# Kernel tuning notes

Hardware: AMD Instinct MI355X
Metric: run time of the kernel (lower is better)

Reference implementation:

```python
import jax, jax.numpy as jnp
import numpy as np

N = 2060          # drug-graph nodes (m_drug_d_num)
F_OUT = 901       # out_feats, forced by Linear(901*2, ...)
M = 901 + (N - 1183)  # 1778 fused node rows
E = N * 64
N_TRAIN, N_TEST = 100000, 30000
EPS = 1e-5


def setup_inputs() -> dict:
    key = jax.random.key(0)
    ks = jax.random.split(key, 30)
    f32 = jnp.float32
    inp = {
        'x_feat': jax.random.normal(ks[0], (N, N), f32),
        'mirna_feat': jax.random.normal(ks[1], (M, F_OUT), f32),
        'Wg': jax.random.normal(ks[2], (N, F_OUT), f32) * 0.02,
        'att_src': jax.random.normal(ks[3], (F_OUT,), f32) * 0.05,
        'att_dst': jax.random.normal(ks[4], (F_OUT,), f32) * 0.05,
        'gat_b': jnp.zeros((F_OUT,), f32),
        'lw1': jax.random.normal(ks[5], (1, 2), f32) * 0.5,
        'lb1': jnp.zeros((1,), f32),
        'lw2': jax.random.normal(ks[6], (2, 1), f32) * 0.5,
        'lb2': jnp.zeros((2,), f32),
        'gw1': jax.random.normal(ks[7], (1, 2), f32) * 0.5,
        'gb1': jnp.zeros((1,), f32),
        'gw2': jax.random.normal(ks[8], (2, 1), f32) * 0.5,
        'gb2': jnp.zeros((2,), f32),
        'W1': jax.random.normal(ks[9], (2 * F_OUT, 1024), f32) * 0.02,
        'b1': jnp.zeros((1024,), f32),
        'W2': jax.random.normal(ks[10], (1024, 512), f32) * 0.03,
        'b2': jnp.zeros((512,), f32),
        'W3': jax.random.normal(ks[11], (512, 64), f32) * 0.04,
        'b3': jnp.zeros((64,), f32),
        'W4': jax.random.normal(ks[12], (64, 1), f32) * 0.1,
        'b4': jnp.zeros((1,), f32),
        'edge_index': jax.random.randint(ks[13], (2, E), 0, N, jnp.int32),
        'train_sample': jax.random.randint(ks[14], (N_TRAIN, 2), 0, M, jnp.int32),
        'test_sample': jax.random.randint(ks[15], (N_TEST, 2), 0, M, jnp.int32),
    }
    return inp


def _bn(x, axes):
    # BatchNorm in train mode (fresh module: gamma=1, beta=0, biased batch var)
    mu = x.mean(axes, keepdims=True)
    var = x.var(axes, keepdims=True)
    return (x - mu) * jax.lax.rsqrt(var + EPS)


def _gat(x, Wg, att_src, att_dst, gat_b, edge_index):
    # single-head PyG-style GATConv with self loops, negative_slope=0.2
    h = x @ Wg                                         # [N, F]
    loop = jnp.arange(N, dtype=edge_index.dtype)
    src = jnp.concatenate([edge_index[0], loop])
    dst = jnp.concatenate([edge_index[1], loop])
    a_s = h @ att_src                                  # [N]
    a_d = h @ att_dst
    e = jax.nn.leaky_relu(a_s[src] + a_d[dst], 0.2)    # per-edge logits
    emax = jax.ops.segment_max(e, dst, num_segments=N)
    ex = jnp.exp(e - emax[dst])
    denom = jax.ops.segment_sum(ex, dst, num_segments=N)
    alpha = ex / denom[dst]
    out = jax.ops.segment_sum(alpha[:, None] * h[src], dst, num_segments=N) + gat_b
    return jax.nn.relu(out)                            # F.relu in MGL (MGC relu is idempotent)


def _forward(x_feat, mirna_feat, Wg, att_src, att_dst, gat_b,
             lw1, lb1, lw2, lb2, gw1, gb1, gw2, gb2,
             W1, b1, W2, b2, W3, b3, W4, b4,
             edge_index, train_sample, test_sample):
    g = _gat(x_feat, Wg, att_src, att_dst, gat_b, edge_index)      # [N, 901]
    drug_view = jnp.concatenate([g[:901], g[1183:]], axis=0)       # [M, 901]
    x = jnp.stack([drug_view, mirna_feat], axis=1)                 # [M, 2, 901]  (B=M, C=2, H=1 dropped, W=901)

    # MS_CAM (channels=2, r=2), BN in train mode
    xl = jnp.einsum('mcw,oc->mow', x, lw1) + lb1[None, :, None]    # [M, 1, 901]
    xl = jax.nn.relu(_bn(xl, (0, 2)))
    xl = jnp.einsum('mcw,oc->mow', xl, lw2) + lb2[None, :, None]   # [M, 2, 901]
    xl = _bn(xl, (0, 2))

    gp = x.mean(axis=2)                                            # [M, 2] global avg pool
    xg = gp @ gw1.T + gb1                                          # [M, 1]
    xg = jax.nn.relu(_bn(xg, (0,)))
    xg = xg @ gw2.T + gb2                                          # [M, 2]
    xg = _bn(xg, (0,))

    wei = jax.nn.sigmoid(xl + xg[:, :, None])
    x = x * wei                                                    # [M, 2, 901]
    fused = (x[:, 0, :] + x[:, 1, :]) * 0.5                        # [M, 901]

    def score(pairs):
        emb = jnp.concatenate([fused[pairs[:, 0]], fused[pairs[:, 1]]], axis=1)  # [B, 1802]
        h = emb @ W1 + b1
        h = h @ W2 + b2
        h = h @ W3 + b3
        return jax.nn.sigmoid(h @ W4 + b4)

    return score(train_sample), score(test_sample)


def reference(x_feat, mirna_feat, Wg, att_src, att_dst, gat_b,
              lw1, lb1, lw2, lb2, gw1, gb1, gw2, gb2,
              W1, b1, W2, b2, W3, b3, W4, b4,
              edge_index, train_sample, test_sample):
    return _forward(x_feat, mirna_feat, Wg, att_src, att_dst, gat_b,
                    lw1, lb1, lw2, lb2, gw1, gb1, gw2, gb2,
                    W1, b1, W2, b2, W3, b3, W4, b4,
                    edge_index, train_sample, test_sample)
```

## Files before the change

### kernel.cpp

```cpp
#include <hip/hip_runtime.h>

typedef unsigned short u16;
typedef unsigned int   u32;

#define NN   2060
#define FF   901
#define HP   904
#define MM   1778
#define EE   131840
#define ETOT 133900
#define NTR  100000
#define NOUT 130000
#define MP   2112
#define KP   2080
#define NP   960
#define EPSV 1e-5f
#define NTOT 1601978.0

typedef __attribute__((ext_vector_type(4))) float f32x4;
typedef __attribute__((ext_vector_type(8))) short bf16x8;

__device__ __forceinline__ float bf2f(u16 u){ return __uint_as_float(((u32)u)<<16); }
__device__ __forceinline__ u16 f2bf(float f){
  u32 b = __float_as_uint(f);
  return (u16)((b + 0x7fffu + ((b>>16)&1u)) >> 16);
}
__device__ __forceinline__ float ldf(const void* p, size_t i, int bf){
  return bf ? bf2f(((const u16*)p)[i]) : ((const float*)p)[i];
}
__device__ __forceinline__ u16 ldb(const void* p, size_t i, int bf){
  return bf ? ((const u16*)p)[i] : f2bf(((const float*)p)[i]);
}
__device__ __forceinline__ float waveSum(float v){
  #pragma unroll
  for (int o = 32; o; o >>= 1) v += __shfl_down(v, o);
  return v;
}
__device__ __forceinline__ int waveSumI(int v){
  #pragma unroll
  for (int o = 32; o; o >>= 1) v += __shfl_down(v, o);
  return v;
}

__global__ __launch_bounds__(64) void probe_k(const u32* __restrict__ x, int* flag){
  int tid = threadIdx.x;
  int big = 0;
  for (int i = tid; i < 128; i += 64){
    u32 w = x[i];
    big += (((w >> 7)  & 0xFFu) >= 0xC0u);
    big += (((w >> 23) & 0xFFu) >= 0xC0u);
  }
  big = waveSumI(big);
  if (tid == 0) *flag = (big >= 8) ? 0 : 1;
}

__global__ __launch_bounds__(256) void padA_k(const void* __restrict__ X, u16* __restrict__ Ap, const int* bfp){
  int bf = *bfp;
  int col = blockIdx.x * 256 + threadIdx.x;
  int row = blockIdx.y;
  if (col >= KP) return;
  u16 v = 0;
  if (row < NN && col < NN) v = ldb(X, (size_t)row * NN + col, bf);
  Ap[(size_t)row * KP + col] = v;
}

__global__ __launch_bounds__(256) void padBT_k(const void* __restrict__ Wg, u16* __restrict__ BT, const int* bfp){
  int bf = *bfp;
  __shared__ u16 t[32][33];
  int kb = blockIdx.x * 32, nb = blockIdx.y * 32;
  int tx = threadIdx.x & 31, ty = threadIdx.x >> 5;
  #pragma unroll
  for (int i = 0; i < 4; ++i){
    int k = kb + ty + 8*i, n = nb + tx;
    u16 v = 0;
    if (k < NN && n < FF) v = ldb(Wg, (size_t)k * FF + n, bf);
    t[ty + 8*i][tx] = v;
  }
  __syncthreads();
  #pragma unroll
  for (int i = 0; i < 4; ++i){
    int n = nb + ty + 8*i, k = kb + tx;
    if (n < NP && k < KP) BT[(size_t)n * KP + k] = t[tx][ty + 8*i];
  }
}

__global__ __launch_bounds__(256) void gemm_k(const u16* __restrict__ A, const u16* __restrict__ BT,
                                              u16* __restrict__ h){
  __shared__ u16 sA[64*32];
  __shared__ u16 sB[64*32];
  int bm = blockIdx.x * 64, bn = blockIdx.y * 64;
  int tid = threadIdx.x, lane = tid & 63, wave = tid >> 6;
  int wm = (wave >> 1) * 32, wn = (wave & 1) * 32;
  f32x4 acc[2][2] = {};
  int sr = tid >> 2, sc = (tid & 3) * 8;
  int fr = lane & 15, quad = lane >> 4;
  const int KIT = KP / 32;
  for (int kt = 0; kt < KIT; ++kt){
    int k0 = kt * 32;
    uint4 va = *(const uint4*)(A  + (size_t)(bm + sr) * KP + k0 + sc);
    uint4 vb = *(const uint4*)(BT + (size_t)(bn + sr) * KP + k0 + sc);
    __syncthreads();
    *(uint4*)&sA[sr*32 + sc] = va;
    *(uint4*)&sB[sr*32 + sc] = vb;
    __syncthreads();
    bf16x8 a0 = *(const bf16x8*)&sA[(wm      + fr)*32 + quad*8];
    bf16x8 a1 = *(const bf16x8*)&sA[(wm + 16 + fr)*32 + quad*8];
    bf16x8 b0 = *(const bf16x8*)&sB[(wn      + fr)*32 + quad*8];
    bf16x8 b1 = *(const bf16x8*)&sB[(wn + 16 + fr)*32 + quad*8];
    acc[0][0] = __builtin_amdgcn_mfma_f32_16x16x32_bf16(a0, b0, acc[0][0], 0,0,0);
    acc[0][1] = __builtin_amdgcn_mfma_f32_16x16x32_bf16(a0, b1, acc[0][1], 0,0,0);
    acc[1][0] = __builtin_amdgcn_mfma_f32_16x16x32_bf16(a1, b0, acc[1][0], 0,0,0);
    acc[1][1] = __builtin_amdgcn_mfma_f32_16x16x32_bf16(a1, b1, acc[1][1], 0,0,0);
  }
  #pragma unroll
  for (int im = 0; im < 2; ++im)
    #pragma unroll
    for (int in = 0; in < 2; ++in)
      #pragma unroll
      for (int i = 0; i < 4; ++i){
        int row = bm + wm + im*16 + quad*4 + i;
        int col = bn + wn + in*16 + fr;
        if (row < NN && col < FF) h[(size_t)row * HP + col] = f2bf(acc[im][in][i]);
      }
}

__global__ __launch_bounds__(64) void asd_k(const u16* __restrict__ h, const void* att_s, const void* att_d,
                                            float* a_s, float* a_d, const int* bfp){
  int bf = *bfp;
  int n = blockIdx.x, tid = threadIdx.x;
  float ss = 0, sd = 0;
  for (int f = tid; f < FF; f += 64){
    float hv = bf2f(h[(size_t)n * HP + f]);
    ss += hv * ldf(att_s, f, bf);
    sd += hv * ldf(att_d, f, bf);
  }
  ss = waveSum(ss); sd = waveSum(sd);
  if (tid == 0){ a_s[n] = ss; a_d[n] = sd; }
}

__global__ __launch_bounds__(256) void edge1_k(const int* __restrict__ ei, const float* __restrict__ a_s,
                                               const float* __restrict__ a_d, float* __restrict__ e_val,
                                               u32* __restrict__ emax, int* __restrict__ counts){
  int e = blockIdx.x * 256 + threadIdx.x;
  if (e >= ETOT) return;
  int src, dst;
  if (e < EE){ src = ei[e]; dst = ei[EE + e]; } else { src = dst = e - EE; }
  float x = a_s[src] + a_d[dst];
  float ev = x > 0.f ? x : 0.2f * x;
  e_val[e] = ev;
  u32 bits = __float_as_uint(ev);
  u32 enc = (bits & 0x80000000u) ? ~bits : (bits | 0x80000000u);
  atomicMax(&emax[dst], enc);
  atomicAdd(&counts[dst], 1);
}

__global__ __launch_bounds__(256) void scan_k(const int* __restrict__ counts, int* __restrict__ offs){
  __shared__ int part[256];
  int tid = threadIdx.x;
  const int CH = (NN + 255) / 256;
  int base = tid * CH, s = 0;
  for (int i = 0; i < CH; ++i){ int idx = base + i; if (idx < NN) s += counts[idx]; }
  part[tid] = s;
  __syncthreads();
  if (tid == 0){ int run = 0; for (int i = 0; i < 256; ++i){ int v = part[i]; part[i] = run; run += v; } }
  __syncthreads();
  int run = part[tid];
  for (int i = 0; i < CH; ++i){ int idx = base + i; if (idx < NN){ offs[idx] = run; run += counts[idx]; } }
  if (tid == 255) offs[NN] = run;
}

__global__ __launch_bounds__(256) void edge2_k(const int* __restrict__ ei, const float* __restrict__ e_val,
                                               const u32* __restrict__ emax, float* __restrict__ denom,
                                               const int* __restrict__ offs, int* __restrict__ fill,
                                               int* __restrict__ csr_src, float* __restrict__ csr_w){
  int e = blockIdx.x * 256 + threadIdx.x;
  if (e >= ETOT) return;
  int src, dst;
  if (e < EE){ src = ei[e]; dst = ei[EE + e]; } else { src = dst = e - EE; }
  u32 enc = emax[dst];
  u32 bits = (enc & 0x80000000u) ? (enc & 0x7fffffffu) : ~enc;
  float ex = expf(e_val[e] - __uint_as_float(bits));
  atomicAdd(&denom[dst], ex);
  int pos = offs[dst] + atomicAdd(&fill[dst], 1);
  csr_src[pos] = src; csr_w[pos] = ex;
}

__global__ __launch_bounds__(256) void aggr_k(const u16* __restrict__ h, const int* __restrict__ offs,
                                              const int* __restrict__ csr_src, const float* __restrict__ csr_w,
                                              const float* __restrict__ denom, const void* gat_b,
                                              float* __restrict__ g, const int* bfp){
  int bf = *bfp;
  int dst = blockIdx.x, tid = threadIdx.x;
  int o0 = offs[dst], o1 = offs[dst + 1];
  float inv = 1.0f / denom[dst];
  __shared__ int   sS[256];
  __shared__ float sW[256];
  const int c = tid;
  float ax = 0, ay = 0, az = 0, aw = 0;
  for (int base = o0; base < o1; base += 256){
    int nb = min(256, o1 - base);
    __syncthreads();
    if (tid < nb){ sS[tid] = csr_src[base + tid]; sW[tid] = csr_w[base + tid] * inv; }
    __syncthreads();
    if (c < 226){
      int k = 0;
      for (; k + 4 <= nb; k += 4){
        int   i0 = sS[k], i1 = sS[k+1], i2 = sS[k+2], i3 = sS[k+3];
        float w0 = sW[k], w1 = sW[k+1], w2 = sW[k+2], w3 = sW[k+3];
        ushort4 v0 = ((const ushort4*)(h + (size_t)i0 * HP))[c];
        ushort4 v1 = ((const ushort4*)(h + (size_t)i1 * HP))[c];
        ushort4 v2 = ((const ushort4*)(h + (size_t)i2 * HP))[c];
        ushort4 v3 = ((const ushort4*)(h + (size_t)i3 * HP))[c];
        ax += w0*bf2f(v0.x) + w1*bf2f(v1.x) + w2*bf2f(v2.x) + w3*bf2f(v3.x);
        ay += w0*bf2f(v0.y) + w1*bf2f(v1.y) + w2*bf2f(v2.y) + w3*bf2f(v3.y);
        az += w0*bf2f(v0.z) + w1*bf2f(v1.z) + w2*bf2f(v2.z) + w3*bf2f(v3.z);
        aw += w0*bf2f(v0.w) + w1*bf2f(v1.w) + w2*bf2f(v2.w) + w3*bf2f(v3.w);
      }
      for (; k < nb; ++k){
        int i0 = sS[k]; float w0 = sW[k];
        ushort4 v0 = ((const ushort4*)(h + (size_t)i0 * HP))[c];
        ax += w0*bf2f(v0.x); ay += w0*bf2f(v0.y); az += w0*bf2f(v0.z); aw += w0*bf2f(v0.w);
      }
    }
  }
  if (c < 226){
    int f0 = 4*c;
    float4 r;
    r.x = ax + ((f0+0) < FF ? ldf(gat_b, f0+0, bf) : 0.f);
    r.y = ay + ((f0+1) < FF ? ldf(gat_b, f0+1, bf) : 0.f);
    r.z = az + ((f0+2) < FF ? ldf(gat_b, f0+2, bf) : 0.f);
    r.w = aw + ((f0+3) < FF ? ldf(gat_b, f0+3, bf) : 0.f);
    r.x = r.x > 0.f ? r.x : 0.f;
    r.y = r.y > 0.f ? r.y : 0.f;
    r.z = r.z > 0.f ? r.z : 0.f;
    r.w = r.w > 0.f ? r.w : 0.f;
    ((float4*)(g + (size_t)dst * HP))[c] = r;
  }
}

__global__ __launch_bounds__(256) void statsA_k(const float* __restrict__ g, const void* __restrict__ mirna,
                                                const void* lw1, const void* lb1,
                                                float* __restrict__ gp, float2* __restrict__ pA, const int* bfp){
  int bf = *bfp;
  int m = blockIdx.x, tid = threadIdx.x;
  int gr = m < 901 ? m : m + 282;
  float w00 = ldf(lw1,0,bf), w01 = ldf(lw1,1,bf), bb = ldf(lb1,0,bf);
  float sx0 = 0, sx1 = 0, sl = 0, sl2 = 0;
  for (int w = tid; w < FF; w += 256){
    float x0 = g[(size_t)gr * HP + w];
    float x1 = ldf(mirna, (size_t)m * FF + w, bf);
    sx0 += x0; sx1 += x1;
    float xl = w00*x0 + w01*x1 + bb;
    sl += xl; sl2 += xl*xl;
  }
  sx0 = waveSum(sx0); sx1 = waveSum(sx1); sl = waveSum(sl); sl2 = waveSum(sl2);
  __shared__ float sh[4][4];
  int wv = tid >> 6;
  if ((tid & 63) == 0){ sh[0][wv]=sx0; sh[1][wv]=sx1; sh[2][wv]=sl; sh[3][wv]=sl2; }
  __syncthreads();
  if (tid == 0){
    float t0 = sh[0][0]+sh[0][1]+sh[0][2]+sh[0][3];
    float t1 = sh[1][0]+sh[1][1]+sh[1][2]+sh[1][3];
    float t2 = sh[2][0]+sh[2][1]+sh[2][2]+sh[2][3];
    float t3 = sh[3][0]+sh[3][1]+sh[3][2]+sh[3][3];
    gp[2*m] = t0 / (float)FF; gp[2*m+1] = t1 / (float)FF;
    pA[m] = make_float2(t2, t3);
  }
}

__global__ __launch_bounds__(256) void xg_k(const float* __restrict__ gp, const void* gw1, const void* gb1,
                                            const void* gw2, float* __restrict__ xg2b,
                                            const float2* __restrict__ pA, double* __restrict__ Sd,
                                            const int* bfp){
  int bf = *bfp;
  __shared__ float xs[MM];
  __shared__ float red[2][4];
  __shared__ float bc[3];
  int tid = threadIdx.x;
  float s = 0, s2 = 0;
  for (int m = tid; m < MM; m += 256){ float2 p = pA[m]; s += p.x; s2 += p.y; }
  s = waveSum(s); s2 = waveSum(s2);
  if ((tid & 63) == 0){ red[0][tid>>6] = s; red[1][tid>>6] = s2; }
  __syncthreads();
  if (tid == 0){
    Sd[0] = (double)(red[0][0]+red[0][1]+red[0][2]+red[0][3]);
    Sd[1] = (double)(red[1][0]+red[1][1]+red[1][2]+red[1][3]);
  }
  __syncthreads();
  float g10 = ldf(gw1,0,bf), g11 = ldf(gw1,1,bf), b1v = ldf(gb1,0,bf);
  s = 0; s2 = 0;
  for (int m = tid; m < MM; m += 256){
    float v = g10*gp[2*m] + g11*gp[2*m+1] + b1v;
    xs[m] = v; s += v; s2 += v*v;
  }
  s = waveSum(s); s2 = waveSum(s2);
  __syncthreads();
  if ((tid & 63) == 0){ red[0][tid>>6] = s; red[1][tid>>6] = s2; }
  __syncthreads();
  if (tid == 0){
    float t  = red[0][0]+red[0][1]+red[0][2]+red[0][3];
    float t2 = red[1][0]+red[1][1]+red[1][2]+red[1][3];
    float mean = t / (float)MM, var = t2 / (float)MM - mean*mean;
    bc[0] = mean; bc[1] = rsqrtf(var + EPSV);
  }
  __syncthreads();
  float mean = bc[0], rs = bc[1];
  s = 0; s2 = 0;
  for (int m = tid; m < MM; m += 256){
    float r = (xs[m] - mean) * rs; r = r > 0.f ? r : 0.f;
    xs[m] = r; s += r; s2 += r*r;
  }
  s = waveSum(s); s2 = waveSum(s2);
  __syncthreads();
  if ((tid & 63) == 0){ red[0][tid>>6] = s; red[1][tid>>6] = s2; }
  __syncthreads();
  if (tid == 0){
    float t  = red[0][0]+red[0][1]+red[0][2]+red[0][3];
    float t2 = red[1][0]+red[1][1]+red[1][2]+red[1][3];
    float mrg = t / (float)MM, vrg = t2 / (float)MM - mrg*mrg;
    float g20 = ldf(gw2,0,bf), g21 = ldf(gw2,1,bf);
    bc[0] = mrg;
    bc[1] = g20 * rsqrtf(g20*g20*vrg + EPSV);
    bc[2] = g21 * rsqrtf(g21*g21*vrg + EPSV);
  }
  __syncthreads();
  float mrg = bc[0], c0 = bc[1], c1 = bc[2];
  for (int m = tid; m < MM; m += 256){
    float d = xs[m] - mrg;
    xg2b[2*m] = c0 * d; xg2b[2*m+1] = c1 * d;
  }
}

__global__ __launch_bounds__(256) void statsB_k(const float* __restrict__ g, const void* __restrict__ mirna,
                                                const void* lw1, const void* lb1,
                                                const double* __restrict__ S, float2* __restrict__ pB,
                                                const int* bfp){
  int bf = *bfp;
  int m = blockIdx.x, tid = threadIdx.x;
  int gr = m < 901 ? m : m + 282;
  float w00 = ldf(lw1,0,bf), w01 = ldf(lw1,1,bf), bb = ldf(lb1,0,bf);
  float mu1 = (float)(S[0] / NTOT);
  float rs1 = rsqrtf((float)(S[1] / NTOT) - mu1*mu1 + EPSV);
  float sr = 0, sr2 = 0;
  for (int w = tid; w < FF; w += 256){
    float x0 = g[(size_t)gr * HP + w];
    float x1 = ldf(mirna, (size_t)m * FF + w, bf);
    float xl = w00*x0 + w01*x1 + bb;
    float r = (xl - mu1) * rs1; r = r > 0.f ? r : 0.f;
    sr += r; sr2 += r*r;
  }
  sr = waveSum(sr); sr2 = waveSum(sr2);
  __shared__ float sh[2][4];
  if ((tid & 63) == 0){ sh[0][tid>>6] = sr; sh[1][tid>>6] = sr2; }
  __syncthreads();
  if (tid == 0) pB[m] = make_float2(sh[0][0]+sh[0][1]+sh[0][2]+sh[0][3],
                                    sh[1][0]+sh[1][1]+sh[1][2]+sh[1][3]);
}

__global__ __launch_bounds__(256) void redB_k(const float2* __restrict__ pB, double* __restrict__ Sd){
  int tid = threadIdx.x;
  float s = 0, s2 = 0;
  for (int m = tid; m < MM; m += 256){ float2 p = pB[m]; s += p.x; s2 += p.y; }
  s = waveSum(s); s2 = waveSum(s2);
  __shared__ float sh[2][4];
  if ((tid & 63) == 0){ sh[0][tid>>6] = s; sh[1][tid>>6] = s2; }
  __syncthreads();
  if (tid == 0){
    Sd[2] = (double)(sh[0][0]+sh[0][1]+sh[0][2]+sh[0][3]);
    Sd[3] = (double)(sh[1][0]+sh[1][1]+sh[1][2]+sh[1][3]);
  }
}

__global__ __launch_bounds__(256) void fs_k(const float* __restrict__ g, const void* __restrict__ mirna,
                                            const void* lw1, const void* lb1, const void* lw2,
                                            const double* __restrict__ S, const float* __restrict__ xg2b,
                                            const float* __restrict__ u1,
                                            float* __restrict__ s0, float* __restrict__ s1, const int* bfp){
  int bf = *bfp;
  int m = blockIdx.x, tid = threadIdx.x;
  int gr = m < 901 ? m : m + 282;
  float w00 = ldf(lw1,0,bf), w01 = ldf(lw1,1,bf), bb = ldf(lb1,0,bf);
  float mu1 = (float)(S[0] / NTOT);
  float rs1 = rsqrtf((float)(S[1] / NTOT) - mu1*mu1 + EPSV);
  float mr  = (float)(S[2] / NTOT);
  float vr  = (float)(S[3] / NTOT) - mr*mr;
  float l20 = ldf(lw2,0,bf), l21 = ldf(lw2,1,bf);
  float A0 = l20 * rsqrtf(l20*l20*vr + EPSV);
  float A1 = l21 * rsqrtf(l21*l21*vr + EPSV);
  float xa = xg2b[2*m], xb = xg2b[2*m+1];
  float p0 = 0, p1 = 0;
  for (int w = tid; w < FF; w += 256){
    float x0 = g[(size_t)gr * HP + w];
    float x1 = ldf(mirna, (size_t)m * FF + w, bf);
    float xl = w00*x0 + w01*x1 + bb;
    float r = (xl - mu1) * rs1; r = r > 0.f ? r : 0.f;
    float rc = r - mr;
    float z0 = A0*rc + xa, z1 = A1*rc + xb;
    float sg0 = 1.f / (1.f + expf(-z0));
    float sg1 = 1.f / (1.f + expf(-z1));
    float f = 0.5f * (x0*sg0 + x1*sg1);
    p0 += f * u1[w]; p1 += f * u1[901 + w];
  }
  p0 = waveSum(p0); p1 = waveSum(p1);
  __shared__ float sh[2][4];
  if ((tid & 63) == 0){ sh[0][tid>>6] = p0; sh[1][tid>>6] = p1; }
  __syncthreads();
  if (tid == 0){
    s0[m] = sh[0][0]+sh[0][1]+sh[0][2]+sh[0][3];
    s1[m] = sh[1][0]+sh[1][1]+sh[1][2]+sh[1][3];
  }
}

__global__ __launch_bounds__(64) void coll1_k(const void* __restrict__ W3, const void* __restrict__ W4,
                                              const void* b3, const void* b4, float* __restrict__ u3,
                                              double* cacc, const int* bfp){
  int bf = *bfp;
  int ob = blockIdx.x, tid = threadIdx.x;
  float s = (ob < 512) ? ldf(W3, ob*64 + tid, bf) * ldf(W4, tid, bf)
                       : ldf(b3, tid, bf) * ldf(W4, tid, bf);
  s = waveSum(s);
  if (tid == 0){
    if (ob < 512) u3[ob] = s;
    else atomicAdd(cacc, (double)(s + ldf(b4, 0, bf)));
  }
}
__global__ __launch_bounds__(256) void coll2_k(const void* __restrict__ W2, const void* __restrict__ b2,
                                               const float* __restrict__ u3, float* __restrict__ u2,
                                               double* cacc, const int* bfp){
  int bf = *bfp;
  int ob = blockIdx.x, tid = threadIdx.x;
  float s = 0;
  if (ob < 1024){
    for (int j = tid; j < 512; j += 256) s += ldf(W2, (size_t)ob * 512 + j, bf) * u3[j];
  } else {
    for (int j = tid; j < 512; j += 256) s += ldf(b2, j, bf) * u3[j];
  }
  s = waveSum(s);
  __shared__ float sh[4];
  if ((tid & 63) == 0) sh[tid>>6] = s;
  __syncthreads();
  if (tid == 0){
    float t = sh[0]+sh[1]+sh[2]+sh[3];
    if (ob < 1024) u2[ob] = t; else atomicAdd(cacc, (double)t);
  }
}
__global__ __launch_bounds__(256) void coll3_k(const void* __restrict__ W1, const void* __restrict__ b1,
                                               const float* __restrict__ u2, float* __restrict__ u1,
                                               double* cacc, const int* bfp){
  int bf = *bfp;
  int ob = blockIdx.x, tid = threadIdx.x;
  float s = 0;
  if (ob < 1802){
    for (int j = tid; j < 1024; j += 256) s += ldf(W1, (size_t)ob * 1024 + j, bf) * u2[j];
  } else {
    for (int j = tid; j < 1024; j += 256) s += ldf(b1, j, bf) * u2[j];
  }
  s = waveSum(s);
  __shared__ float sh[4];
  if ((tid & 63) == 0) sh[tid>>6] = s;
  __syncthreads();
  if (tid == 0){
    float t = sh[0]+sh[1]+sh[2]+sh[3];
    if (ob < 1802) u1[ob] = t; else atomicAdd(cacc, (double)t);
  }
}

__global__ __launch_bounds__(256) void out_k(const int* __restrict__ tr, const int* __restrict__ te,
                                             const float* __restrict__ s0, const float* __restrict__ s1,
                                             const double* __restrict__ cacc, void* __restrict__ out,
                                             const int* bfp){
  int bf = *bfp;
  int b = blockIdx.x * 256 + threadIdx.x;
  if (b >= NOUT) return;
  int i, j;
  if (b < NTR){ i = tr[2*b]; j = tr[2*b + 1]; }
  else { int t = b - NTR; i = te[2*t]; j = te[2*t + 1]; }
  float z = s0[i] + s1[j] + (float)cacc[0];
  float v = 1.f / (1.f + expf(-z));
  if (bf) ((u16*)out)[b] = f2bf(v);
  else    ((float*)out)[b] = v;
}

extern "C" void kernel_launch(void* const* d_in, const int* in_sizes, int n_in,
                              void* d_out, int out_size, void* d_ws, size_t ws_size,
                              hipStream_t stream){
  const void* x_feat = d_in[0];
  const void* mirna  = d_in[1];
  const void* Wg     = d_in[2];
  const void* att_s  = d_in[3];
  const void* att_d  = d_in[4];
  const void* gat_b  = d_in[5];
  const void* lw1    = d_in[6];
  const void* lb1    = d_in[7];
  const void* lw2    = d_in[8];
  const void* gw1    = d_in[10];
  const void* gb1    = d_in[11];
  const void* gw2    = d_in[12];
  const void* W1     = d_in[14];
  const void* b1     = d_in[15];
  const void* W2     = d_in[16];
  const void* b2     = d_in[17];
  const void* W3     = d_in[18];
  const void* b3     = d_in[19];
  const void* W4     = d_in[20];
  const void* b4     = d_in[21];
  const int* ei      = (const int*)d_in[22];
  const int* tr      = (const int*)d_in[23];
  const int* te      = (const int*)d_in[24];

  char* ws = (char*)d_ws;
  size_t off = 0;
  auto alloc = [&](size_t bytes)->size_t{ size_t o = off; off += (bytes + 255) & ~(size_t)255; return o; };
  size_t oA  = alloc((size_t)MP*KP*2);
  size_t oBT = alloc((size_t)NP*KP*2);
  size_t oH  = alloc((size_t)NN*HP*2);
  size_t oEV = alloc((size_t)ETOT*4);
  size_t oCS = alloc((size_t)ETOT*4);
  size_t oCW = alloc((size_t)ETOT*4);
  size_t oAS = alloc(NN*4);
  size_t oAD = alloc(NN*4);
  size_t oOF = alloc((NN+1)*4);
  size_t oGP = alloc(MM*2*4);
  size_t oXG = alloc(MM*2*4);
  size_t oS0 = alloc(MM*4);
  size_t oS1 = alloc(MM*4);
  size_t oU3 = alloc(512*4);
  size_t oU2 = alloc(1024*4);
  size_t oU1 = alloc(1802*4);
  size_t oPA = alloc(MM*8);
  size_t oPB = alloc(MM*8);
  size_t oSS = alloc(4*8);
  size_t oBF = alloc(4);
  size_t zstart = off;
  size_t oC  = alloc(8);
  size_t oMX = alloc(NN*4);
  size_t oDN = alloc(NN*4);
  size_t oCT = alloc(NN*4);
  size_t oFL = alloc(NN*4);
  size_t zend = off;

  u16*   Ap   = (u16*)(ws+oA);
  u16*   BT   = (u16*)(ws+oBT);
  u16*   h    = (u16*)(ws+oH);
  float* gbuf = (float*)(ws+oA);
  float* e_val= (float*)(ws+oEV);
  int*   csrS = (int*)(ws+oCS);
  float* csrW = (float*)(ws+oCW);
  float* a_s  = (float*)(ws+oAS);
  float* a_d  = (float*)(ws+oAD);
  int*   offs = (int*)(ws+oOF);
  float* gp   = (float*)(ws+oGP);
  float* xg2b = (float*)(ws+oXG);
  float* s0   = (float*)(ws+oS0);
  float* s1   = (float*)(ws+oS1);
  float* u3   = (float*)(ws+oU3);
  float* u2   = (float*)(ws+oU2);
  float* u1   = (float*)(ws+oU1);
  float2* pA  = (float2*)(ws+oPA);
  float2* pB  = (float2*)(ws+oPB);
  double* Sd  = (double*)(ws+oSS);
  int*   bfp  = (int*)(ws+oBF);
  double* cacc= (double*)(ws+oC);
  u32*   emax = (u32*)(ws+oMX);
  float* denom= (float*)(ws+oDN);
  int*   cnts = (int*)(ws+oCT);
  int*   fill = (int*)(ws+oFL);

  hipMemsetAsync(ws + zstart, 0, zend - zstart, stream);

  probe_k<<<1, 64, 0, stream>>>((const u32*)x_feat, bfp);
  padA_k <<<dim3((KP+255)/256, MP), 256, 0, stream>>>(x_feat, Ap, bfp);
  padBT_k<<<dim3(KP/32, NP/32),    256, 0, stream>>>(Wg, BT, bfp);
  coll1_k<<<513,  64,  0, stream>>>(W3, W4, b3, b4, u3, cacc, bfp);
  coll2_k<<<1025, 256, 0, stream>>>(W2, b2, u3, u2, cacc, bfp);
  coll3_k<<<1803, 256, 0, stream>>>(W1, b1, u2, u1, cacc, bfp);
  gemm_k <<<dim3(MP/64, NP/64), 256, 0, stream>>>(Ap, BT, h);
  asd_k  <<<NN, 64, 0, stream>>>(h, att_s, att_d, a_s, a_d, bfp);
  edge1_k<<<(ETOT+255)/256, 256, 0, stream>>>(ei, a_s, a_d, e_val, emax, cnts);
  scan_k <<<1, 256, 0, stream>>>(cnts, offs);
  edge2_k<<<(ETOT+255)/256, 256, 0, stream>>>(ei, e_val, emax, denom, offs, fill, csrS, csrW);
  aggr_k <<<NN, 256, 0, stream>>>(h, offs, csrS, csrW, denom, gat_b, gbuf, bfp);
  statsA_k<<<MM, 256, 0, stream>>>(gbuf, mirna, lw1, lb1, gp, pA, bfp);
  xg_k   <<<1, 256, 0, stream>>>(gp, gw1, gb1, gw2, xg2b, pA, Sd, bfp);
  statsB_k<<<MM, 256, 0, stream>>>(gbuf, mirna, lw1, lb1, Sd, pB, bfp);
  redB_k <<<1, 256, 0, stream>>>(pB, Sd);
  fs_k   <<<MM, 256, 0, stream>>>(gbuf, mirna, lw1, lb1, lw2, Sd, xg2b, u1, s0, s1, bfp);
  out_k  <<<(NOUT+255)/256, 256, 0, stream>>>(tr, te, s0, s1, cacc, d_out, bfp);
}
```

Measured before the change: 287.5 us.

## Fuse probe/pad kernels, use direct global-to-LDS loads in GEMM, widen aggregation loads

Merges the dtype probe and both padding kernels into one launch, with each wave recomputing the bf16 flag locally. The GEMM now loads tiles straight into LDS via global_load_lds with an XOR-swizzled chunk layout, avoiding register staging and LDS bank conflicts. The GAT aggregation uses 128 threads with 16-byte loads and 8 accumulators per thread. Together these cut launch count and memory instruction overhead, at the cost of redundant flag reads per block and reliance on the LDS-direct load builtin.

```diff
diff --git a/kernel.cpp b/kernel.cpp
--- a/kernel.cpp
+++ b/kernel.cpp
@@ -20,6 +20,10 @@
 typedef __attribute__((ext_vector_type(4))) float f32x4;
 typedef __attribute__((ext_vector_type(8))) short bf16x8;
 
+#define GLL16(g,l) __builtin_amdgcn_global_load_lds( \
+    (const __attribute__((address_space(1))) u32*)(g), \
+    (__attribute__((address_space(3))) u32*)(l), 16, 0, 0)
+
 __device__ __forceinline__ float bf2f(u16 u){ return __uint_as_float(((u32)u)<<16); }
 __device__ __forceinline__ u16 f2bf(float f){
   u32 b = __float_as_uint(f);
@@ -41,72 +45,78 @@
   for (int o = 32; o; o >>= 1) v += __shfl_down(v, o);
   return v;
 }
-
-__global__ __launch_bounds__(64) void probe_k(const u32* __restrict__ x, int* flag){
-  int tid = threadIdx.x;
-  int big = 0;
-  for (int i = tid; i < 128; i += 64){
-    u32 w = x[i];
-    big += (((w >> 7)  & 0xFFu) >= 0xC0u);
-    big += (((w >> 23) & 0xFFu) >= 0xC0u);
-  }
+__device__ __forceinline__ int flagWave(const u32* __restrict__ x){
+  int l = threadIdx.x & 63;
+  u32 w0 = x[l], w1 = x[l + 64];
+  int big = (((w0 >> 7)  & 0xFFu) >= 0xC0u) + (((w0 >> 23) & 0xFFu) >= 0xC0u)
+          + (((w1 >> 7)  & 0xFFu) >= 0xC0u) + (((w1 >> 23) & 0xFFu) >= 0xC0u);
   big = waveSumI(big);
-  if (tid == 0) *flag = (big >= 8) ? 0 : 1;
-}
-
-__global__ __launch_bounds__(256) void padA_k(const void* __restrict__ X, u16* __restrict__ Ap, const int* bfp){
-  int bf = *bfp;
-  int col = blockIdx.x * 256 + threadIdx.x;
-  int row = blockIdx.y;
-  if (col >= KP) return;
-  u16 v = 0;
-  if (row < NN && col < NN) v = ldb(X, (size_t)row * NN + col, bf);
-  Ap[(size_t)row * KP + col] = v;
-}
-
-__global__ __launch_bounds__(256) void padBT_k(const void* __restrict__ Wg, u16* __restrict__ BT, const int* bfp){
-  int bf = *bfp;
-  __shared__ u16 t[32][33];
-  int kb = blockIdx.x * 32, nb = blockIdx.y * 32;
-  int tx = threadIdx.x & 31, ty = threadIdx.x >> 5;
-  #pragma unroll
-  for (int i = 0; i < 4; ++i){
-    int k = kb + ty + 8*i, n = nb + tx;
+  return (__shfl(big, 0) >= 8) ? 0 : 1;
+}
+
+__global__ __launch_bounds__(256) void pad_k(const void* __restrict__ X, const void* __restrict__ Wg,
+                                             u16* __restrict__ Ap, u16* __restrict__ BT, int* bfp){
+  __shared__ u16 tt[32][33];
+  int bf = flagWave((const u32*)X);
+  int bx = blockIdx.x, by = blockIdx.y, tid = threadIdx.x;
+  if (bx == 0 && by == 0 && tid == 0) *bfp = bf;
+  if (by < MP){
+    int col = bx * 256 + tid, row = by;
+    if (col >= KP) return;
     u16 v = 0;
-    if (k < NN && n < FF) v = ldb(Wg, (size_t)k * FF + n, bf);
-    t[ty + 8*i][tx] = v;
-  }
-  __syncthreads();
-  #pragma unroll
-  for (int i = 0; i < 4; ++i){
-    int n = nb + ty + 8*i, k = kb + tx;
-    if (n < NP && k < KP) BT[(size_t)n * KP + k] = t[tx][ty + 8*i];
+    if (row < NN && col < NN) v = ldb(X, (size_t)row * NN + col, bf);
+    Ap[(size_t)row * KP + col] = v;
+  } else {
+    if (bx) return;
+    int t = by - MP;
+    int kb = (t % 65) * 32, nb = (t / 65) * 32;
+    int tx = tid & 31, ty = tid >> 5;
+    #pragma unroll
+    for (int i = 0; i < 4; ++i){
+      int k = kb + ty + 8*i, n = nb + tx;
+      u16 v = 0;
+      if (k < NN && n < FF) v = ldb(Wg, (size_t)k * FF + n, bf);
+      tt[ty + 8*i][tx] = v;
+    }
+    __syncthreads();
+    #pragma unroll
+    for (int i = 0; i < 4; ++i){
+      int n = nb + ty + 8*i, k = kb + tx;
+      if (n < NP && k < KP) BT[(size_t)n * KP + k] = tt[tx][ty + 8*i];
+    }
   }
 }
 
 __global__ __launch_bounds__(256) void gemm_k(const u16* __restrict__ A, const u16* __restrict__ BT,
                                               u16* __restrict__ h){
-  __shared__ u16 sA[64*32];
-  __shared__ u16 sB[64*32];
+  __shared__ __align__(16) u16 sA[64*32];
+  __shared__ __align__(16) u16 sB[64*32];
   int bm = blockIdx.x * 64, bn = blockIdx.y * 64;
   int tid = threadIdx.x, lane = tid & 63, wave = tid >> 6;
   int wm = (wave >> 1) * 32, wn = (wave & 1) * 32;
   f32x4 acc[2][2] = {};
-  int sr = tid >> 2, sc = (tid & 3) * 8;
+  int srow = tid >> 2;
+  int schunk = (tid & 3) ^ ((tid >> 3) & 3);
+  const u16* gA = A  + (size_t)(bm + srow) * KP + schunk * 8;
+  const u16* gB = BT + (size_t)(bn + srow) * KP + schunk * 8;
+  u16* lA = sA + wave * 512;
+  u16* lB = sB + wave * 512;
   int fr = lane & 15, quad = lane >> 4;
+  int qs = quad ^ ((fr >> 1) & 3);
+  const u16* pa0 = &sA[(wm      + fr) * 32 + qs * 8];
+  const u16* pa1 = &sA[(wm + 16 + fr) * 32 + qs * 8];
+  const u16* pb0 = &sB[(wn      + fr) * 32 + qs * 8];
+  const u16* pb1 = &sB[(wn + 16 + fr) * 32 + qs * 8];
   const int KIT = KP / 32;
   for (int kt = 0; kt < KIT; ++kt){
-    int k0 = kt * 32;
-    uint4 va = *(const uint4*)(A  + (size_t)(bm + sr) * KP + k0 + sc);
-    uint4 vb = *(const uint4*)(BT + (size_t)(bn + sr) * KP + k0 + sc);
     __syncthreads();
-    *(uint4*)&sA[sr*32 + sc] = va;
-    *(uint4*)&sB[sr*32 + sc] = vb;
+    GLL16(gA + kt * 32, lA);
+    GLL16(gB + kt * 32, lB);
     __syncthreads();
-    bf16x8 a0 = *(const bf16x8*)&sA[(wm      + fr)*32 + quad*8];
-    bf16x8 a1 = *(const bf16x8*)&sA[(wm + 16 + fr)*32 + quad*8];
-    bf16x8 b0 = *(const bf16x8*)&sB[(wn      + fr)*32 + quad*8];
-    bf16x8 b1 = *(const bf16x8*)&sB[(wn + 16 + fr)*32 + quad*8];
+    bf16x8 a0 = *(const bf16x8*)pa0;
+    bf16x8 a1 = *(const bf16x8*)pa1;
+    bf16x8 b0 = *(const bf16x8*)pb0;
+    bf16x8 b1 = *(const bf16x8*)pb1;
     acc[0][0] = __builtin_amdgcn_mfma_f32_16x16x32_bf16(a0, b0, acc[0][0], 0,0,0);
     acc[0][1] = __builtin_amdgcn_mfma_f32_16x16x32_bf16(a0, b1, acc[0][1], 0,0,0);
     acc[1][0] = __builtin_amdgcn_mfma_f32_16x16x32_bf16(a1, b0, acc[1][0], 0,0,0);
@@ -185,7 +195,15 @@
   csr_src[pos] = src; csr_w[pos] = ex;
 }
 
-__global__ __launch_bounds__(256) void aggr_k(const u16* __restrict__ h, const int* __restrict__ offs,
+__device__ __forceinline__ void acc8(float* a, uint4 v, float w){
+  u32 arr[4] = {v.x, v.y, v.z, v.w};
+  #pragma unroll
+  for (int i = 0; i < 4; ++i){
+    a[2*i]   += w * __uint_as_float((arr[i] & 0xFFFFu) << 16);
+    a[2*i+1] += w * __uint_as_float(arr[i] & 0xFFFF0000u);
+  }
+}
+__global__ __launch_bounds__(128) void aggr_k(const u16* __restrict__ h, const int* __restrict__ offs,
                                               const int* __restrict__ csr_src, const float* __restrict__ csr_w,
                                               const float* __restrict__ denom, const void* gat_b,
                                               float* __restrict__ g, const int* bfp){
@@ -193,48 +211,43 @@
   int dst = blockIdx.x, tid = threadIdx.x;
   int o0 = offs[dst], o1 = offs[dst + 1];
   float inv = 1.0f / denom[dst];
-  __shared__ int   sS[256];
-  __shared__ float sW[256];
+  __shared__ int   sS[128];
+  __shared__ float sW[128];
   const int c = tid;
-  float ax = 0, ay = 0, az = 0, aw = 0;
-  for (int base = o0; base < o1; base += 256){
-    int nb = min(256, o1 - base);
+  float a[8] = {0,0,0,0,0,0,0,0};
+  for (int base = o0; base < o1; base += 128){
+    int nb = min(128, o1 - base);
     __syncthreads();
     if (tid < nb){ sS[tid] = csr_src[base + tid]; sW[tid] = csr_w[base + tid] * inv; }
     __syncthreads();
-    if (c < 226){
+    if (c < 113){
       int k = 0;
       for (; k + 4 <= nb; k += 4){
         int   i0 = sS[k], i1 = sS[k+1], i2 = sS[k+2], i3 = sS[k+3];
         float w0 = sW[k], w1 = sW[k+1], w2 = sW[k+2], w3 = sW[k+3];
-        ushort4 v0 = ((const ushort4*)(h + (size_t)i0 * HP))[c];
-        ushort4 v1 = ((const ushort4*)(h + (size_t)i1 * HP))[c];
-        ushort4 v2 = ((const ushort4*)(h + (size_t)i2 * HP))[c];
-        ushort4 v3 = ((const ushort4*)(h + (size_t)i3 * HP))[c];
-        ax += w0*bf2f(v0.x) + w1*bf2f(v1.x) + w2*bf2f(v2.x) + w3*bf2f(v3.x);
-        ay += w0*bf2f(v0.y) + w1*bf2f(v1.y) + w2*bf2f(v2.y) + w3*bf2f(v3.y);
-        az += w0*bf2f(v0.z) + w1*bf2f(v1.z) + w2*bf2f(v2.z) + w3*bf2f(v3.z);
-        aw += w0*bf2f(v0.w) + w1*bf2f(v1.w) + w2*bf2f(v2.w) + w3*bf2f(v3.w);
+        uint4 v0 = ((const uint4*)(h + (size_t)i0 * HP))[c];
+        uint4 v1 = ((const uint4*)(h + (size_t)i1 * HP))[c];
+        uint4 v2 = ((const uint4*)(h + (size_t)i2 * HP))[c];
+        uint4 v3 = ((const uint4*)(h + (size_t)i3 * HP))[c];
+        acc8(a, v0, w0); acc8(a, v1, w1); acc8(a, v2, w2); acc8(a, v3, w3);
       }
       for (; k < nb; ++k){
-        int i0 = sS[k]; float w0 = sW[k];
-        ushort4 v0 = ((const ushort4*)(h + (size_t)i0 * HP))[c];
-        ax += w0*bf2f(v0.x); ay += w0*bf2f(v0.y); az += w0*bf2f(v0.z); aw += w0*bf2f(v0.w);
+        uint4 v0 = ((const uint4*)(h + (size_t)sS[k] * HP))[c];
+        acc8(a, v0, sW[k]);
       }
     }
   }
-  if (c < 226){
-    int f0 = 4*c;
-    float4 r;
-    r.x = ax + ((f0+0) < FF ? ldf(gat_b, f0+0, bf) : 0.f);
-    r.y = ay + ((f0+1) < FF ? ldf(gat_b, f0+1, bf) : 0.f);
-    r.z = az + ((f0+2) < FF ? ldf(gat_b, f0+2, bf) : 0.f);
-    r.w = aw + ((f0+3) < FF ? ldf(gat_b, f0+3, bf) : 0.f);
-    r.x = r.x > 0.f ? r.x : 0.f;
-    r.y = r.y > 0.f ? r.y : 0.f;
-    r.z = r.z > 0.f ? r.z : 0.f;
-    r.w = r.w > 0.f ? r.w : 0.f;
-    ((float4*)(g + (size_t)dst * HP))[c] = r;
+  if (c < 113){
+    int f0 = 8 * c;
+    float r[8];
+    #pragma unroll
+    for (int i = 0; i < 8; ++i){
+      float v = a[i] + ((f0 + i) < FF ? ldf(gat_b, f0 + i, bf) : 0.f);
+      r[i] = v > 0.f ? v : 0.f;
+    }
+    float4* go = (float4*)(g + (size_t)dst * HP);
+    go[2*c]   = make_float4(r[0], r[1], r[2], r[3]);
+    go[2*c+1] = make_float4(r[4], r[5], r[6], r[7]);
   }
 }
 
@@ -568,9 +581,7 @@
 
   hipMemsetAsync(ws + zstart, 0, zend - zstart, stream);
 
-  probe_k<<<1, 64, 0, stream>>>((const u32*)x_feat, bfp);
-  padA_k <<<dim3((KP+255)/256, MP), 256, 0, stream>>>(x_feat, Ap, bfp);
-  padBT_k<<<dim3(KP/32, NP/32),    256, 0, stream>>>(Wg, BT, bfp);
+  pad_k  <<<dim3(9, MP + 65*30), 256, 0, stream>>>(x_feat, Wg, Ap, BT, bfp);
   coll1_k<<<513,  64,  0, stream>>>(W3, W4, b3, b4, u3, cacc, bfp);
   coll2_k<<<1025, 256, 0, stream>>>(W2, b2, u3, u2, cacc, bfp);
   coll3_k<<<1803, 256, 0, stream>>>(W1, b1, u2, u1, cacc, bfp);
@@ -579,7 +590,7 @@
   edge1_k<<<(ETOT+255)/256, 256, 0, stream>>>(ei, a_s, a_d, e_val, emax, cnts);
   scan_k <<<1, 256, 0, stream>>>(cnts, offs);
   edge2_k<<<(ETOT+255)/256, 256, 0, stream>>>(ei, e_val, emax, denom, offs, fill, csrS, csrW);
-  aggr_k <<<NN, 256, 0, stream>>>(h, offs, csrS, csrW, denom, gat_b, gbuf, bfp);
+  aggr_k <<<NN, 128, 0, stream>>>(h, offs, csrS, csrW, denom, gat_b, gbuf, bfp);
   statsA_k<<<MM, 256, 0, stream>>>(gbuf, mirna, lw1, lb1, gp, pA, bfp);
   xg_k   <<<1, 256, 0, stream>>>(gp, gw1, gb1, gw2, xg2b, pA, Sd, bfp);
   statsB_k<<<MM, 256, 0, stream>>>(gbuf, mirna, lw1, lb1, Sd, pB, bfp);
```

Measured after the change: 286.6 us. No clear change (-0.3%).
